# Performance work log

Hardware: AMD Instinct MI355X
Metric: run time of the kernel (lower is better)

## Reference

```python
import jax, jax.numpy as jnp
import numpy as np

B, N_PER, K = 8, 4096, 16          # graphs, nodes per graph, knn neighbors
D_IN, D_H, D_OUT = 32, 64, 128     # feature_nn: 35->64->64, global_nn: 64->128
N = B * N_PER


def setup_inputs() -> dict:
    key = jax.random.key(0)
    ks = jax.random.split(key, 8)
    sc = lambda fan: 1.0 / np.sqrt(fan)
    x = jax.random.normal(ks[0], (N, D_IN), jnp.float32)
    pos = jax.random.normal(ks[1], (N, 3), jnp.float32)
    batch = jnp.repeat(jnp.arange(B, dtype=jnp.int32), N_PER)
    fW1 = jax.random.normal(ks[2], (D_IN + 3, D_H), jnp.float32) * sc(D_IN + 3)
    fb1 = jnp.zeros((D_H,), jnp.float32)
    fW2 = jax.random.normal(ks[3], (D_H, D_H), jnp.float32) * sc(D_H)
    fb2 = jnp.zeros((D_H,), jnp.float32)
    gW = jax.random.normal(ks[4], (D_H, D_OUT), jnp.float32) * sc(D_H)
    gb = jnp.zeros((D_OUT,), jnp.float32)
    return {"x": x, "pos": pos, "batch": batch,
            "fW1": fW1, "fb1": fb1, "fW2": fW2, "fb2": fb2,
            "gW": gW, "gb": gb}


def reference(x, pos, batch, fW1, fb1, fW2, fb2, gW, gb):
    # ---- knn(pos, pos, k, batch, batch): per-graph k nearest (self included) ----
    posb = pos.reshape(B, N_PER, 3)
    sq = jnp.sum(posb * posb, axis=-1)                      # [B, Nper]
    dist = sq[:, :, None] + sq[:, None, :] - 2.0 * jnp.einsum('bnd,bmd->bnm', posb, posb)
    _, nbr = jax.lax.top_k(-dist, K)                        # [B, Nper, K] local neighbor idx
    offs = (jnp.arange(B, dtype=nbr.dtype) * N_PER)[:, None, None]
    col = (nbr + offs).reshape(-1)                          # edge_index[1]: neighbor (x) idx
    row = jnp.repeat(jnp.arange(N, dtype=col.dtype), K)     # edge_index[0]: query (y) idx

    # ---- PointConv: msg = feature_nn(cat[x_j, pos_j - pos_i]), max-aggregate at i ----
    # PyG flow source_to_target: j = edge_index[0] = row (query), i = edge_index[1] = col.
    msg = jnp.concatenate([x[row], pos[row] - pos[col]], axis=1)  # [E, 35]
    h = jax.nn.relu(msg @ fW1 + fb1)
    h = jax.nn.relu(h @ fW2 + fb2)                          # [E, 64]
    agg = jax.ops.segment_max(h, col, num_segments=N)       # max aggregation
    agg = jnp.where(jnp.isfinite(agg), agg, 0.0)            # PyG fills empty segments with 0
    out = jax.nn.relu(agg @ gW + gb)                        # global_nn
    return (out, pos, batch)
```

## Files before the change

### kernel.cpp

```cpp
#include <hip/hip_runtime.h>
#include <hip/hip_bf16.h>

#define N_PER    4096
#define KNBR     16
#define NTOT     32768
#define D_IN     32
#define D_H      64
#define D_OUT    128
#define E_TOT    (NTOT * KNBR)

#define OUT1_OFF (NTOT * D_OUT)
#define OUT2_OFF (NTOT * D_OUT + NTOT*3)

#define KNN_INF 3.4e38f

typedef __attribute__((ext_vector_type(8))) short bf16x8;
typedef __attribute__((ext_vector_type(4))) float f32x4;

__device__ float          g_posf[NTOT * 3];
__device__ float          g_scf[NTOT];
__device__ float4         g_pos4[NTOT];
__device__ int            g_nbr[E_TOT];
__device__ unsigned short g_base1h[NTOT * D_H];
__device__ uint4          g_Bfrag[2 * 4 * 64];
__device__ float          g_Wd[3 * D_H];
__device__ float          g_fb2v[D_H];
__device__ int            g_cnt[NTOT];
__device__ int            g_bsum[NTOT / 256];
__device__ int            g_offs[NTOT + 1];
__device__ int            g_cursor[NTOT];
__device__ int            g_inlist[E_TOT];
__device__ float          g_agg[NTOT * D_H];

__device__ __forceinline__ float ldf(const void* p, int i, int bf) {
    if (bf) return __uint_as_float(((unsigned)((const unsigned short*)p)[i]) << 16);
    return ((const float*)p)[i];
}
__device__ __forceinline__ unsigned bf16rne(float f) {
    unsigned u = __float_as_uint(f);
    return (u + 0x7FFFu + ((u >> 16) & 1u)) >> 16;
}
__device__ __forceinline__ void stf(void* p, int i, float v, int bf) {
    if (bf) ((unsigned short*)p)[i] = (unsigned short)bf16rne(v);
    else    ((float*)p)[i] = v;
}
__device__ __forceinline__ float b2f(unsigned short h) {
    return __uint_as_float(((unsigned)h) << 16);
}
__device__ __forceinline__ int wave_probe(const void* x) {
    unsigned wv = ((const unsigned*)x)[threadIdx.x & 63];
    unsigned e = (wv >> 7) & 0xFFu;
    unsigned long long mk = __ballot(e >= 110u && e <= 140u);
    return (__popcll(mk) >= 32) ? 1 : 0;
}

__global__ __launch_bounds__(256) void prep_kernel(const void* __restrict__ x,
                                                   const void* __restrict__ pos,
                                                   const void* __restrict__ fW1,
                                                   const void* __restrict__ fb1,
                                                   const void* __restrict__ fW2,
                                                   const void* __restrict__ fb2) {
    const int bf = wave_probe(x);
    const int b = blockIdx.x;
    if (b < 1024) {
        const int i0 = b * 256 + threadIdx.x;
        const int stride = 1024 * 256;
        for (int i = i0; i < NTOT * 3; i += stride) g_posf[i] = ldf(pos, i, bf);
        {
#pragma clang fp contract(off)
            for (int i = i0; i < NTOT; i += stride) {
                float a = ldf(pos, i * 3 + 0, bf);
                float c2 = ldf(pos, i * 3 + 1, bf);
                float c3 = ldf(pos, i * 3 + 2, bf);
                float sc = a * a + c2 * c2 + c3 * c3;
                g_scf[i] = sc;
                g_pos4[i] = make_float4(-2.0f * a, -2.0f * c2, -2.0f * c3, sc);
                g_cnt[i] = 0;
            }
        }
        for (int i = i0; i < NTOT * D_H; i += stride) g_agg[i] = 0.0f;
    } else if (b < 2048) {
        int lane = threadIdx.x & 63, wid = threadIdx.x >> 6;
        int n0 = (b - 1024) * 32 + wid * 8;
        float wcol[D_IN];
#pragma unroll
        for (int k = 0; k < D_IN; k++) wcol[k] = ldf(fW1, k * D_H + lane, bf);
        float bb = ldf(fb1, lane, bf);
        if (bf) {
            const unsigned short* xp = (const unsigned short*)x;
            for (int r = 0; r < 8; r++) {
                int n = n0 + r;
                const uint4* xr = (const uint4*)(xp + (size_t)n * D_IN);
                float acc = bb;
#pragma unroll
                for (int q4 = 0; q4 < 4; q4++) {
                    uint4 w4 = xr[q4];
                    unsigned ww[4] = {w4.x, w4.y, w4.z, w4.w};
#pragma unroll
                    for (int p = 0; p < 4; p++) {
                        int k = q4 * 8 + p * 2;
                        acc += __uint_as_float(ww[p] << 16) * wcol[k];
                        acc += __uint_as_float(ww[p] & 0xFFFF0000u) * wcol[k + 1];
                    }
                }
                g_base1h[(size_t)n * D_H + lane] = (unsigned short)bf16rne(acc);
            }
        } else {
            const float* xp = (const float*)x;
            for (int r = 0; r < 8; r++) {
                int n = n0 + r;
                const float4* xr = (const float4*)(xp + (size_t)n * D_IN);
                float acc = bb;
#pragma unroll
                for (int q4 = 0; q4 < 8; q4++) {
                    float4 w4 = xr[q4];
                    int k = q4 * 4;
                    acc += w4.x * wcol[k] + w4.y * wcol[k + 1] + w4.z * wcol[k + 2] + w4.w * wcol[k + 3];
                }
                g_base1h[(size_t)n * D_H + lane] = (unsigned short)bf16rne(acc);
            }
        }
    } else {
        for (int t = threadIdx.x; t < 3 * D_H; t += 256) g_Wd[t] = ldf(fW1, D_IN * D_H + t, bf);
        if (threadIdx.x < D_H) g_fb2v[threadIdx.x] = ldf(fb2, threadIdx.x, bf);
        for (int idx = threadIdx.x; idx < 512; idx += 256) {
            int lane = idx & 63, nt = (idx >> 6) & 3, ks = idx >> 8;
            int n = nt * 16 + (lane & 15);
            int k0 = ks * 32 + ((lane >> 4) << 3);
            unsigned wds[4];
#pragma unroll
            for (int jp = 0; jp < 4; jp++) {
                unsigned lo = bf16rne(ldf(fW2, (k0 + 2 * jp) * D_H + n, bf));
                unsigned hi = bf16rne(ldf(fW2, (k0 + 2 * jp + 1) * D_H + n, bf));
                wds[jp] = lo | (hi << 16);
            }
            g_Bfrag[idx] = make_uint4(wds[0], wds[1], wds[2], wds[3]);
        }
    }
}

__global__ __launch_bounds__(512) void knn_kernel() {
#pragma clang fp contract(off)
    __shared__ float4 s_c4[2048];
    __shared__ int s_i[8][8][64];
    const int lane = threadIdx.x & 63;
    const int wid  = threadIdx.x >> 6;
    const int qbase = blockIdx.x * 64 + wid * 8;
    const int cbase = (qbase >> 12) << 12;
    const float* cp  = g_posf + cbase * 3;
    const float* csc = g_scf + cbase;

    float qx[8], qy[8], qz[8], qs[8];
#pragma unroll
    for (int r = 0; r < 8; r++) {
        qx[r] = g_posf[(qbase + r) * 3 + 0];
        qy[r] = g_posf[(qbase + r) * 3 + 1];
        qz[r] = g_posf[(qbase + r) * 3 + 2];
        qs[r] = g_scf[qbase + r];
    }

    float m[8];
#pragma unroll
    for (int r = 0; r < 8; r++) m[r] = KNN_INF;
    for (int ch = 0; ch < 2; ch++) {
        __syncthreads();
        const float4* gp = g_pos4 + cbase + ch * 2048;
        for (int i = threadIdx.x; i < 2048; i += 512) s_c4[i] = gp[i];
        __syncthreads();
#pragma unroll 4
        for (int c = 0; c < 32; c++) {
            float4 v4 = s_c4[c * 64 + lane];
#pragma unroll
            for (int r = 0; r < 8; r++) {
                float d = fmaf(v4.z, qz[r], fmaf(v4.y, qy[r], fmaf(v4.x, qx[r], v4.w)));
                m[r] = fminf(m[r], d);
            }
        }
    }

    float T[8];
#pragma unroll
    for (int r = 0; r < 8; r++) {
        float v = m[r];
#pragma unroll
        for (int k = 2; k <= 64; k <<= 1) {
#pragma unroll
            for (int j2 = k >> 1; j2 >= 1; j2 >>= 1) {
                float pv = __shfl_xor(v, j2);
                bool keepMin = (((lane & j2) == 0) == ((lane & k) == 0));
                bool tp = ((pv < v) == keepMin);
                v = tp ? pv : v;
            }
        }
        T[r] = __shfl(v, 15) + 1e-3f;
    }

    int cnt[8];
#pragma unroll
    for (int r = 0; r < 8; r++) cnt[r] = 0;
    for (int ch = 0; ch < 2; ch++) {
        __syncthreads();
        const float4* gp = g_pos4 + cbase + ch * 2048;
        for (int i = threadIdx.x; i < 2048; i += 512) s_c4[i] = gp[i];
        __syncthreads();
        for (int c = 0; c < 32; c++) {
            int jj = c * 64 + lane;
            float4 v4 = s_c4[jj];
#pragma unroll
            for (int r = 0; r < 8; r++) {
                float d = fmaf(v4.z, qz[r], fmaf(v4.y, qy[r], fmaf(v4.x, qx[r], v4.w)));
                bool p = (d <= T[r]);
                unsigned long long mk = __ballot(p);
                if (mk) {
                    int pre = (int)__popcll(mk & ((1ull << lane) - 1ull));
                    int slot = cnt[r] + pre;
                    if (p && slot < 64) s_i[wid][r][slot] = cbase + ch * 2048 + jj;
                    cnt[r] += (int)__popcll(mk);
                }
            }
        }
    }

#pragma unroll
    for (int r = 0; r < 8; r++) {
        int q = qbase + r;
        if (cnt[r] <= 64) {
            int S = cnt[r];
            int idx = (lane < S) ? s_i[wid][r][lane] : 0x7FFFFFFF;
            float d = KNN_INF;
            if (lane < S) {
                float px = g_posf[idx * 3], py = g_posf[idx * 3 + 1], pz = g_posf[idx * 3 + 2];
                float sc = g_scf[idx];
                float dot = px * qx[r] + py * qy[r] + pz * qz[r];
                d = (qs[r] + sc) - 2.0f * dot;
            }
#pragma unroll
            for (int k = 2; k <= 64; k <<= 1) {
#pragma unroll
                for (int j2 = k >> 1; j2 >= 1; j2 >>= 1) {
                    float pd = __shfl_xor(d, j2);
                    int   pi = __shfl_xor(idx, j2);
                    bool keepMin = (((lane & j2) == 0) == ((lane & k) == 0));
                    bool lt = (pd < d) || (pd == d && pi < idx);
                    bool tp = (lt == keepMin);
                    d   = tp ? pd : d;
                    idx = tp ? pi : idx;
                }
            }
            if (lane < 16) {
                g_nbr[q * KNBR + lane] = idx;
                atomicAdd(&g_cnt[idx & (NTOT - 1)], 1);
            }
        } else {
            float lastd = -KNN_INF; int lasti = -1;
            for (int t = 0; t < 16; t++) {
                float bd = KNN_INF; int bi = 0x7FFFFFFF;
                for (int c = 0; c < 64; c++) {
                    int jj = c * 64 + lane;
                    float px = cp[jj * 3], py = cp[jj * 3 + 1], pz = cp[jj * 3 + 2];
                    float sc = csc[jj];
                    float dot = px * qx[r] + py * qy[r] + pz * qz[r];
                    float dd = (qs[r] + sc) - 2.0f * dot;
                    int gj = cbase + jj;
                    bool after  = (dd > lastd) || (dd == lastd && gj > lasti);
                    bool better = (dd < bd) || (dd == bd && gj < bi);
                    if (after && better) { bd = dd; bi = gj; }
                }
#pragma unroll
                for (int s2 = 1; s2 < 64; s2 <<= 1) {
                    float od = __shfl_xor(bd, s2);
                    int   oi = __shfl_xor(bi, s2);
                    if (od < bd || (od == bd && oi < bi)) { bd = od; bi = oi; }
                }
                if (lane == 0) {
                    g_nbr[q * KNBR + t] = bi;
                    atomicAdd(&g_cnt[bi & (NTOT - 1)], 1);
                }
                lastd = bd; lasti = bi;
            }
        }
    }
}

__global__ __launch_bounds__(256) void scanA_kernel() {
    __shared__ int red[4];
    int t = threadIdx.x, lane = t & 63, w = t >> 6;
    int v = g_cnt[blockIdx.x * 256 + t];
    int s = v;
#pragma unroll
    for (int off = 1; off < 64; off <<= 1) s += __shfl_xor(s, off);
    if (lane == 0) red[w] = s;
    __syncthreads();
    if (t == 0) g_bsum[blockIdx.x] = red[0] + red[1] + red[2] + red[3];
}

__global__ __launch_bounds__(256) void scanC_kernel() {
    __shared__ int sred[4];
    __shared__ int wsum[4];
    int t = threadIdx.x, lane = t & 63, w = t >> 6;
    int contrib = (t < 128 && t < blockIdx.x) ? g_bsum[t] : 0;
    int rs = contrib;
#pragma unroll
    for (int off = 1; off < 64; off <<= 1) rs += __shfl_xor(rs, off);
    if (lane == 0) sred[w] = rs;
    __syncthreads();
    int base = sred[0] + sred[1] + sred[2] + sred[3];

    int i = blockIdx.x * 256 + t;
    int v = g_cnt[i];
    int inc = v;
#pragma unroll
    for (int off = 1; off < 64; off <<= 1) {
        int u = __shfl_up(inc, off);
        if (lane >= off) inc += u;
    }
    if (lane == 63) wsum[w] = inc;
    __syncthreads();
    int wbase = 0;
    for (int k = 0; k < w; k++) wbase += wsum[k];
    int excl = base + wbase + inc - v;
    g_offs[i] = excl;
    g_cursor[i] = excl;
    if (i == NTOT - 1) g_offs[NTOT] = E_TOT;
}

__global__ void scatter_kernel() {
    int e = blockIdx.x * 256 + threadIdx.x;
    int c = g_nbr[e] & (NTOT - 1);
    int slot = atomicAdd(&g_cursor[c], 1);
    g_inlist[slot & (E_TOT - 1)] = e;
}

__global__ __launch_bounds__(256) void edge_kernel() {
    __shared__ unsigned short sA[256 * 72];
    __shared__ int scol[256];
    const int t    = threadIdx.x;
    const int lane = t & 63;
    const int w    = t >> 6;
    const int slot0 = blockIdx.x * 256;

    {
        int e = g_inlist[slot0 + t];
        int n = (e >> 4) & (NTOT - 1);
        int j = g_nbr[e] & (NTOT - 1);
        scol[t] = j;
        float dx = g_posf[n * 3 + 0] - g_posf[j * 3 + 0];
        float dy = g_posf[n * 3 + 1] - g_posf[j * 3 + 1];
        float dz = g_posf[n * 3 + 2] - g_posf[j * 3 + 2];
        const unsigned short* b1 = g_base1h + (size_t)n * D_H;
#pragma unroll
        for (int d0 = 0; d0 < D_H; d0 += 8) {
            uint4 p = *(const uint4*)(b1 + d0);
            unsigned pw[4] = {p.x, p.y, p.z, p.w};
            unsigned qw[4];
#pragma unroll
            for (int jp = 0; jp < 4; jp++) {
                int d = d0 + 2 * jp;
                float v0 = __uint_as_float(pw[jp] << 16)
                         + dx * g_Wd[d]     + dy * g_Wd[64 + d]     + dz * g_Wd[128 + d];
                float v1 = __uint_as_float(pw[jp] & 0xFFFF0000u)
                         + dx * g_Wd[d + 1] + dy * g_Wd[64 + d + 1] + dz * g_Wd[128 + d + 1];
                v0 = fmaxf(v0, 0.f); v1 = fmaxf(v1, 0.f);
                qw[jp] = bf16rne(v0) | (bf16rne(v1) << 16);
            }
            *(uint4*)(&sA[t * 72 + d0]) = make_uint4(qw[0], qw[1], qw[2], qw[3]);
        }
    }
    __syncthreads();

    f32x4 acc[4][4];
#pragma unroll
    for (int a = 0; a < 4; a++)
#pragma unroll
        for (int b = 0; b < 4; b++) acc[a][b] = (f32x4){0.f, 0.f, 0.f, 0.f};

    const int quad = lane >> 4;
    const int l15  = lane & 15;
#pragma unroll
    for (int ks = 0; ks < 2; ks++) {
        bf16x8 bfrag[4];
#pragma unroll
        for (int nt = 0; nt < 4; nt++)
            bfrag[nt] = ((const bf16x8*)g_Bfrag)[ks * 256 + nt * 64 + lane];
#pragma unroll
        for (int mt = 0; mt < 4; mt++) {
            int row = w * 64 + mt * 16 + l15;
            bf16x8 afrag = *(const bf16x8*)(&sA[row * 72 + ks * 32 + quad * 8]);
#pragma unroll
            for (int nt = 0; nt < 4; nt++)
                acc[mt][nt] = __builtin_amdgcn_mfma_f32_16x16x32_bf16(afrag, bfrag[nt], acc[mt][nt], 0, 0, 0);
        }
    }
    __syncthreads();

#pragma unroll
    for (int nt = 0; nt < 4; nt++) {
        int dim = nt * 16 + l15;
        float bb = g_fb2v[dim];
#pragma unroll
        for (int mt = 0; mt < 4; mt++) {
#pragma unroll
            for (int r = 0; r < 4; r++) {
                int edge = w * 64 + mt * 16 + quad * 4 + r;
                float v = fmaxf(acc[mt][nt][r] + bb, 0.f);
                sA[edge * 72 + dim] = (unsigned short)bf16rne(v);
            }
        }
    }
    __syncthreads();

    {
        const int ls0 = w * 64;
        const int gs0 = slot0 + ls0;
        int cur = -1;
        float vmax = 0.f;
        for (int s = ls0; s < ls0 + 64; s++) {
            int cj = scol[s];
            float v = b2f(sA[s * 72 + lane]);
            if (cj != cur) {
                if (cur >= 0) {
                    int lo = g_offs[cur], hi = g_offs[cur + 1];
                    if (lo >= gs0 && hi <= gs0 + 64)
                        g_agg[(size_t)cur * D_H + lane] = vmax;
                    else
                        atomicMax((unsigned*)&g_agg[(size_t)cur * D_H + lane], __float_as_uint(vmax));
                }
                cur = cj; vmax = v;
            } else {
                vmax = fmaxf(vmax, v);
            }
        }
        if (cur >= 0) {
            int lo = g_offs[cur], hi = g_offs[cur + 1];
            if (lo >= gs0 && hi <= gs0 + 64)
                g_agg[(size_t)cur * D_H + lane] = vmax;
            else
                atomicMax((unsigned*)&g_agg[(size_t)cur * D_H + lane], __float_as_uint(vmax));
        }
    }
}

__global__ __launch_bounds__(256) void outmisc_kernel(const void* __restrict__ x,
                                                      const void* __restrict__ gW,
                                                      const void* __restrict__ gb,
                                                      const int* __restrict__ batch,
                                                      const void* __restrict__ pos,
                                                      void* __restrict__ out) {
    const int bf = wave_probe(x);
    const int b = blockIdx.x;
    if (b < 2048) {
        int t = threadIdx.x, d = t & 127, half = t >> 7;
        float gcol[D_H];
#pragma unroll
        for (int k = 0; k < D_H; k++) gcol[k] = ldf(gW, k * D_OUT + d, bf);
        float bb = ldf(gb, d, bf);
        int n0 = b * 16 + half * 8;
        for (int r = 0; r < 8; r++) {
            int n = n0 + r;
            float acc = bb;
#pragma unroll
            for (int k = 0; k < D_H; k++) acc += g_agg[(size_t)n * D_H + k] * gcol[k];
            stf(out, n * D_OUT + d, fmaxf(acc, 0.f), bf);
        }
    } else {
        int i = (b - 2048) * 256 + threadIdx.x;
        if (bf) {
            if (i < NTOT * 3) ((unsigned short*)out)[OUT1_OFF + i] = ((const unsigned short*)pos)[i];
            if (i < NTOT)     ((unsigned short*)out)[OUT2_OFF + i] = (unsigned short)bf16rne((float)batch[i]);
        } else {
            if (i < NTOT * 3) ((float*)out)[OUT1_OFF + i] = ((const float*)pos)[i];
            if (i < NTOT)     ((float*)out)[OUT2_OFF + i] = (float)batch[i];
        }
    }
}

extern "C" void kernel_launch(void* const* d_in, const int* in_sizes, int n_in,
                              void* d_out, int out_size, void* d_ws, size_t ws_size,
                              hipStream_t stream) {
    const void* x     = d_in[0];
    const void* pos   = d_in[1];
    const int*  batch = (const int*)d_in[2];
    const void* fW1   = d_in[3];
    const void* fb1   = d_in[4];
    const void* fW2   = d_in[5];
    const void* fb2   = d_in[6];
    const void* gW    = d_in[7];
    const void* gb    = d_in[8];

    hipLaunchKernelGGL(prep_kernel,    dim3(2049),        dim3(256), 0, stream, x, pos, fW1, fb1, fW2, fb2);
    hipLaunchKernelGGL(knn_kernel,     dim3(NTOT / 64),   dim3(512), 0, stream);
    hipLaunchKernelGGL(scanA_kernel,   dim3(NTOT / 256),  dim3(256), 0, stream);
    hipLaunchKernelGGL(scanC_kernel,   dim3(NTOT / 256),  dim3(256), 0, stream);
    hipLaunchKernelGGL(scatter_kernel, dim3(E_TOT / 256), dim3(256), 0, stream);
    hipLaunchKernelGGL(edge_kernel,    dim3(E_TOT / 256), dim3(256), 0, stream);
    hipLaunchKernelGGL(outmisc_kernel, dim3(2048 + (NTOT * 3 + 255) / 256), dim3(256), 0, stream,
                       x, gW, gb, batch, pos, d_out);
}
```

Measured before the change: 269.1 us.

## Compute kNN distance screening with split-bf16 MFMA instead of scalar FMAs

Positions and squared norms are packed as hi/lo bf16 pairs, so each query-candidate distance comes from a 32x32x16 bf16 MFMA rather than per-lane scalar FMAs. The threshold pass and candidate collection now run on MFMA tiles, with per-query minima merged through shared memory and candidate lists built with shared atomics. Exact fp32 distances still rank the survivors, and the threshold margin is widened to absorb bf16 error. The cost is more shared memory and a per-element ballot in the collection pass, and lists can overflow into the slow fallback more often.

```diff
diff --git a/kernel.cpp b/kernel.cpp
--- a/kernel.cpp
+++ b/kernel.cpp
@@ -12,14 +12,17 @@
 #define OUT1_OFF (NTOT * D_OUT)
 #define OUT2_OFF (NTOT * D_OUT + NTOT*3)
 
-#define KNN_INF 3.4e38f
-
-typedef __attribute__((ext_vector_type(8))) short bf16x8;
-typedef __attribute__((ext_vector_type(4))) float f32x4;
+#define KNN_INF    3.4e38f
+#define KNN_MARGIN 4e-3f
+
+typedef __attribute__((ext_vector_type(8)))  short bf16x8;
+typedef __attribute__((ext_vector_type(4)))  float f32x4;
+typedef __attribute__((ext_vector_type(16))) float f32x16;
 
 __device__ float          g_posf[NTOT * 3];
 __device__ float          g_scf[NTOT];
-__device__ float4         g_pos4[NTOT];
+__device__ __attribute__((aligned(16))) unsigned short g_knnA[NTOT * 16];
+__device__ __attribute__((aligned(16))) unsigned short g_knnB[NTOT * 16];
 __device__ int            g_nbr[E_TOT];
 __device__ unsigned short g_base1h[NTOT * D_H];
 __device__ uint4          g_Bfrag[2 * 4 * 64];
@@ -69,13 +72,28 @@
         {
 #pragma clang fp contract(off)
             for (int i = i0; i < NTOT; i += stride) {
-                float a = ldf(pos, i * 3 + 0, bf);
+                float a  = ldf(pos, i * 3 + 0, bf);
                 float c2 = ldf(pos, i * 3 + 1, bf);
                 float c3 = ldf(pos, i * 3 + 2, bf);
                 float sc = a * a + c2 * c2 + c3 * c3;
                 g_scf[i] = sc;
-                g_pos4[i] = make_float4(-2.0f * a, -2.0f * c2, -2.0f * c3, sc);
                 g_cnt[i] = 0;
+                unsigned hx = bf16rne(a),  hy = bf16rne(c2), hz = bf16rne(c3);
+                float fhx = b2f(hx), fhy = b2f(hy), fhz = b2f(hz);
+                unsigned lx = bf16rne(a - fhx), ly = bf16rne(c2 - fhy), lz = bf16rne(c3 - fhz);
+                unsigned sch = bf16rne(sc);
+                unsigned scl = bf16rne(sc - b2f(sch));
+                unsigned nx = bf16rne(-2.0f * fhx), ny = bf16rne(-2.0f * fhy), nz = bf16rne(-2.0f * fhz);
+                unsigned ox = bf16rne(-2.0f * b2f(lx)), oy = bf16rne(-2.0f * b2f(ly)), oz = bf16rne(-2.0f * b2f(lz));
+                const unsigned ONEB = 0x3F80u;
+                uint4 A0 = make_uint4(nx | (ny << 16), nz | (ox << 16), oy | (oz << 16), nx | (ny << 16));
+                uint4 A1 = make_uint4(nz | (ONEB << 16), ONEB, 0u, 0u);
+                uint4 B0 = make_uint4(hx | (hy << 16), hz | (hx << 16), hy | (hz << 16), lx | (ly << 16));
+                uint4 B1 = make_uint4(lz | (sch << 16), scl, 0u, 0u);
+                *(uint4*)&g_knnA[(size_t)i * 16]     = A0;
+                *(uint4*)&g_knnA[(size_t)i * 16 + 8] = A1;
+                *(uint4*)&g_knnB[(size_t)i * 16]     = B0;
+                *(uint4*)&g_knnB[(size_t)i * 16 + 8] = B1;
             }
         }
         for (int i = i0; i < NTOT * D_H; i += stride) g_agg[i] = 0.0f;
@@ -139,128 +157,178 @@
     }
 }
 
+__device__ __forceinline__ void knn_sortval(float& v, int lane) {
+#pragma unroll
+    for (int k = 2; k <= 64; k <<= 1) {
+#pragma unroll
+        for (int j2 = k >> 1; j2 >= 1; j2 >>= 1) {
+            float pv = __shfl_xor(v, j2);
+            bool keepMin = (((lane & j2) == 0) == ((lane & k) == 0));
+            bool tp = ((pv < v) == keepMin);
+            v = tp ? pv : v;
+        }
+    }
+}
+__device__ __forceinline__ void knn_sortpair(float& d, int& idx, int lane) {
+#pragma unroll
+    for (int k = 2; k <= 64; k <<= 1) {
+#pragma unroll
+        for (int j2 = k >> 1; j2 >= 1; j2 >>= 1) {
+            float pd = __shfl_xor(d, j2);
+            int   pi = __shfl_xor(idx, j2);
+            bool keepMin = (((lane & j2) == 0) == ((lane & k) == 0));
+            bool lt = (pd < d) || (pd == d && pi < idx);
+            bool tp = (lt == keepMin);
+            d   = tp ? pd : d;
+            idx = tp ? pi : idx;
+        }
+    }
+}
+
 __global__ __launch_bounds__(512) void knn_kernel() {
 #pragma clang fp contract(off)
-    __shared__ float4 s_c4[2048];
-    __shared__ int s_i[8][8][64];
-    const int lane = threadIdx.x & 63;
-    const int wid  = threadIdx.x >> 6;
-    const int qbase = blockIdx.x * 64 + wid * 8;
-    const int cbase = (qbase >> 12) << 12;
-    const float* cp  = g_posf + cbase * 3;
-    const float* csc = g_scf + cbase;
-
-    float qx[8], qy[8], qz[8], qs[8];
-#pragma unroll
-    for (int r = 0; r < 8; r++) {
-        qx[r] = g_posf[(qbase + r) * 3 + 0];
-        qy[r] = g_posf[(qbase + r) * 3 + 1];
-        qz[r] = g_posf[(qbase + r) * 3 + 2];
-        qs[r] = g_scf[qbase + r];
-    }
-
-    float m[8];
-#pragma unroll
-    for (int r = 0; r < 8; r++) m[r] = KNN_INF;
-    for (int ch = 0; ch < 2; ch++) {
-        __syncthreads();
-        const float4* gp = g_pos4 + cbase + ch * 2048;
-        for (int i = threadIdx.x; i < 2048; i += 512) s_c4[i] = gp[i];
-        __syncthreads();
-#pragma unroll 4
-        for (int c = 0; c < 32; c++) {
-            float4 v4 = s_c4[c * 64 + lane];
-#pragma unroll
-            for (int r = 0; r < 8; r++) {
-                float d = fmaf(v4.z, qz[r], fmaf(v4.y, qy[r], fmaf(v4.x, qx[r], v4.w)));
-                m[r] = fminf(m[r], d);
-            }
-        }
-    }
-
-    float T[8];
-#pragma unroll
-    for (int r = 0; r < 8; r++) {
-        float v = m[r];
-#pragma unroll
-        for (int k = 2; k <= 64; k <<= 1) {
-#pragma unroll
-            for (int j2 = k >> 1; j2 >= 1; j2 >>= 1) {
-                float pv = __shfl_xor(v, j2);
-                bool keepMin = (((lane & j2) == 0) == ((lane & k) == 0));
-                bool tp = ((pv < v) == keepMin);
-                v = tp ? pv : v;
-            }
-        }
-        T[r] = __shfl(v, 15) + 1e-3f;
-    }
-
-    int cnt[8];
-#pragma unroll
-    for (int r = 0; r < 8; r++) cnt[r] = 0;
-    for (int ch = 0; ch < 2; ch++) {
-        __syncthreads();
-        const float4* gp = g_pos4 + cbase + ch * 2048;
-        for (int i = threadIdx.x; i < 2048; i += 512) s_c4[i] = gp[i];
-        __syncthreads();
-        for (int c = 0; c < 32; c++) {
-            int jj = c * 64 + lane;
-            float4 v4 = s_c4[jj];
-#pragma unroll
-            for (int r = 0; r < 8; r++) {
-                float d = fmaf(v4.z, qz[r], fmaf(v4.y, qy[r], fmaf(v4.x, qx[r], v4.w)));
-                bool p = (d <= T[r]);
-                unsigned long long mk = __ballot(p);
-                if (mk) {
-                    int pre = (int)__popcll(mk & ((1ull << lane) - 1ull));
-                    int slot = cnt[r] + pre;
-                    if (p && slot < 64) s_i[wid][r][slot] = cbase + ch * 2048 + jj;
-                    cnt[r] += (int)__popcll(mk);
-                }
-            }
-        }
-    }
-
-#pragma unroll
-    for (int r = 0; r < 8; r++) {
-        int q = qbase + r;
-        if (cnt[r] <= 64) {
-            int S = cnt[r];
-            int idx = (lane < S) ? s_i[wid][r][lane] : 0x7FFFFFFF;
+    __shared__ float          s_min[64][128];
+    __shared__ float          s_T[64];
+    __shared__ int            s_cnt[64];
+    __shared__ unsigned short s_list[64][64];
+
+    const int t       = threadIdx.x;
+    const int lane    = t & 63;
+    const int w       = t >> 6;
+    const int mtile   = w & 1;
+    const int quarter = w >> 1;
+    const int half    = lane >> 5;
+    const int col     = lane & 31;
+    const int qbase   = blockIdx.x * 64;
+    const int cbase   = (qbase >> 12) << 12;
+
+    if (t < 64) s_cnt[t] = 0;
+
+    const int qrow = qbase + mtile * 32 + col;
+    const bf16x8 afrag = *(const bf16x8*)&g_knnA[(size_t)qrow * 16 + half * 8];
+    const unsigned short* bp = g_knnB + (size_t)(cbase + quarter * 1024 + col) * 16 + half * 8;
+
+    const f32x16 z = {};
+
+    float m[16];
+#pragma unroll
+    for (int i = 0; i < 16; i++) m[i] = KNN_INF;
+    {
+        bf16x8 nb0 = *(const bf16x8*)(bp + 0 * 512);
+        bf16x8 nb1 = *(const bf16x8*)(bp + 1 * 512);
+        bf16x8 nb2 = *(const bf16x8*)(bp + 2 * 512);
+        bf16x8 nb3 = *(const bf16x8*)(bp + 3 * 512);
+        for (int g = 0; g < 8; g++) {
+            bf16x8 cb0 = nb0, cb1 = nb1, cb2 = nb2, cb3 = nb3;
+            if (g < 7) {
+                const unsigned short* np = bp + (g + 1) * 2048;
+                nb0 = *(const bf16x8*)(np + 0 * 512);
+                nb1 = *(const bf16x8*)(np + 1 * 512);
+                nb2 = *(const bf16x8*)(np + 2 * 512);
+                nb3 = *(const bf16x8*)(np + 3 * 512);
+            }
+            f32x16 c0 = __builtin_amdgcn_mfma_f32_32x32x16_bf16(afrag, cb0, z, 0, 0, 0);
+            f32x16 c1 = __builtin_amdgcn_mfma_f32_32x32x16_bf16(afrag, cb1, z, 0, 0, 0);
+            f32x16 c2 = __builtin_amdgcn_mfma_f32_32x32x16_bf16(afrag, cb2, z, 0, 0, 0);
+            f32x16 c3 = __builtin_amdgcn_mfma_f32_32x32x16_bf16(afrag, cb3, z, 0, 0, 0);
+#pragma unroll
+            for (int i = 0; i < 16; i++)
+                m[i] = fminf(m[i], fminf(fminf(c0[i], c1[i]), fminf(c2[i], c3[i])));
+        }
+    }
+#pragma unroll
+    for (int i = 0; i < 16; i++) {
+        int row = (i & 3) + 8 * (i >> 2) + 4 * half;
+        s_min[mtile * 32 + row][quarter * 32 + col] = m[i];
+    }
+    __syncthreads();
+
+    for (int it = 0; it < 8; it++) {
+        int q = w * 8 + it;
+        float v = fminf(s_min[q][lane], s_min[q][64 + lane]);
+        knn_sortval(v, lane);
+        if (lane == 15) s_T[q] = v + KNN_MARGIN;
+    }
+    __syncthreads();
+
+    float Treg[16];
+#pragma unroll
+    for (int i = 0; i < 16; i++) {
+        int row = (i & 3) + 8 * (i >> 2) + 4 * half;
+        Treg[i] = s_T[mtile * 32 + row];
+    }
+    {
+        bf16x8 nb0 = *(const bf16x8*)(bp + 0 * 512);
+        bf16x8 nb1 = *(const bf16x8*)(bp + 1 * 512);
+        bf16x8 nb2 = *(const bf16x8*)(bp + 2 * 512);
+        bf16x8 nb3 = *(const bf16x8*)(bp + 3 * 512);
+        for (int g = 0; g < 8; g++) {
+            bf16x8 cb[4] = {nb0, nb1, nb2, nb3};
+            if (g < 7) {
+                const unsigned short* np = bp + (g + 1) * 2048;
+                nb0 = *(const bf16x8*)(np + 0 * 512);
+                nb1 = *(const bf16x8*)(np + 1 * 512);
+                nb2 = *(const bf16x8*)(np + 2 * 512);
+                nb3 = *(const bf16x8*)(np + 3 * 512);
+            }
+#pragma unroll
+            for (int u = 0; u < 4; u++) {
+                f32x16 c = __builtin_amdgcn_mfma_f32_32x32x16_bf16(afrag, cb[u], z, 0, 0, 0);
+                int lc = quarter * 1024 + (g * 4 + u) * 32 + col;
+#pragma unroll
+                for (int i = 0; i < 16; i++) {
+                    bool p = (c[i] <= Treg[i]);
+                    unsigned long long mk = __ballot(p);
+                    if (mk) {
+                        int q = mtile * 32 + (i & 3) + 8 * (i >> 2) + 4 * half;
+                        unsigned mk32 = (unsigned)(mk >> (half * 32));
+                        int base = 0;
+                        if (col == 0) base = atomicAdd(&s_cnt[q], __popc(mk32));
+                        base = __shfl(base, half * 32);
+                        if (p) {
+                            int slot = base + __popc(mk32 & ((1u << col) - 1u));
+                            if (slot < 64) s_list[q][slot] = (unsigned short)lc;
+                        }
+                    }
+                }
+            }
+        }
+    }
+    __syncthreads();
+
+    for (int it = 0; it < 8; it++) {
+        int ql = w * 8 + it;
+        int q  = qbase + ql;
+        float qx = g_posf[q * 3 + 0], qy = g_posf[q * 3 + 1], qz = g_posf[q * 3 + 2];
+        float qs = g_scf[q];
+        int S = s_cnt[ql];
+        if (S <= 64) {
+            int idx = 0x7FFFFFFF;
             float d = KNN_INF;
             if (lane < S) {
+                idx = cbase + (int)s_list[ql][lane];
                 float px = g_posf[idx * 3], py = g_posf[idx * 3 + 1], pz = g_posf[idx * 3 + 2];
                 float sc = g_scf[idx];
-                float dot = px * qx[r] + py * qy[r] + pz * qz[r];
-                d = (qs[r] + sc) - 2.0f * dot;
-            }
-#pragma unroll
-            for (int k = 2; k <= 64; k <<= 1) {
-#pragma unroll
-                for (int j2 = k >> 1; j2 >= 1; j2 >>= 1) {
-                    float pd = __shfl_xor(d, j2);
-                    int   pi = __shfl_xor(idx, j2);
-                    bool keepMin = (((lane & j2) == 0) == ((lane & k) == 0));
-                    bool lt = (pd < d) || (pd == d && pi < idx);
-                    bool tp = (lt == keepMin);
-                    d   = tp ? pd : d;
-                    idx = tp ? pi : idx;
-                }
-            }
+                float dot = px * qx + py * qy + pz * qz;
+                d = (qs + sc) - 2.0f * dot;
+            }
+            knn_sortpair(d, idx, lane);
             if (lane < 16) {
                 g_nbr[q * KNBR + lane] = idx;
                 atomicAdd(&g_cnt[idx & (NTOT - 1)], 1);
             }
         } else {
+            const float* cp  = g_posf + cbase * 3;
+            const float* csc = g_scf + cbase;
             float lastd = -KNN_INF; int lasti = -1;
-            for (int t = 0; t < 16; t++) {
+            for (int t16 = 0; t16 < 16; t16++) {
                 float bd = KNN_INF; int bi = 0x7FFFFFFF;
-                for (int c = 0; c < 64; c++) {
-                    int jj = c * 64 + lane;
+                for (int cc = 0; cc < 64; cc++) {
+                    int jj = cc * 64 + lane;
                     float px = cp[jj * 3], py = cp[jj * 3 + 1], pz = cp[jj * 3 + 2];
                     float sc = csc[jj];
-                    float dot = px * qx[r] + py * qy[r] + pz * qz[r];
-                    float dd = (qs[r] + sc) - 2.0f * dot;
+                    float dot = px * qx + py * qy + pz * qz;
+                    float dd = (qs + sc) - 2.0f * dot;
                     int gj = cbase + jj;
                     bool after  = (dd > lastd) || (dd == lastd && gj > lasti);
                     bool better = (dd < bd) || (dd == bd && gj < bi);
@@ -273,7 +341,7 @@
                     if (od < bd || (od == bd && oi < bi)) { bd = od; bi = oi; }
                 }
                 if (lane == 0) {
-                    g_nbr[q * KNBR + t] = bi;
+                    g_nbr[q * KNBR + t16] = bi;
                     atomicAdd(&g_cnt[bi & (NTOT - 1)], 1);
                 }
                 lastd = bd; lasti = bi;
```

New measurement: 272.1 us. About the same (+1.1%).
